# Kernel tuning notes

Hardware: AMD Instinct MI355X
Metric: run time of the kernel (lower is better)

The kernel has to match this reference:

```python
import jax, jax.numpy as jnp
import numpy as np

HID, H, DK, DV, PQK, PV = 128, 12, 16, 16, 4, 8
N, L = 4, 1024


def setup_inputs() -> dict:
    key = jax.random.key(0)
    ks = jax.random.split(key, 12)
    inp = {
        "x": jax.random.normal(ks[0], (N, L, HID), jnp.float32),
        "R": jax.random.normal(ks[1], (N, L, 3, 3), jnp.float32),
        "t": jax.random.normal(ks[2], (N, L, 3), jnp.float32),
        "mask": jnp.ones((N, L), dtype=bool),
        # Linear weights stored as (in, out) so y = x @ W
        "Wq": jax.random.normal(ks[3], (HID, H * DK), jnp.float32) * 0.05,
        "Wk": jax.random.normal(ks[4], (HID, H * DK), jnp.float32) * 0.05,
        "Wv": jax.random.normal(ks[5], (HID, H * DV), jnp.float32) * 0.05,
        "Wqv": jax.random.normal(ks[6], (HID, H * PQK * 3), jnp.float32) * 0.05,
        "Wkv": jax.random.normal(ks[7], (HID, H * PQK * 3), jnp.float32) * 0.05,
        "Wvv": jax.random.normal(ks[8], (HID, H * PV * 3), jnp.float32) * 0.05,
        "gamma": jax.random.normal(ks[9], (H,), jnp.float32) * 0.1,
        "Wo": jax.random.normal(ks[10], (H * (DV + PV * 4), HID), jnp.float32) * 0.05,
        "bo": jnp.zeros((HID,), jnp.float32),
    }
    return inp


def reference(x, R, t, mask, Wq, Wk, Wv, Wqv, Wkv, Wvv, gamma, Wo, bo):
    n, l, _ = x.shape
    q = (x @ Wq).reshape(n, l, H, DK)
    k = (x @ Wk).reshape(n, l, H, DK)
    # standard scores: (N,H,L,L)
    scores = jnp.einsum("bihd,bjhd->bhij", q, k) * DK ** -0.5

    q_vec = (x @ Wqv).reshape(n, l, H, PQK, 3)
    k_vec = (x @ Wkv).reshape(n, l, H, PQK, 3)
    # apply frame: R @ v + t, per residue i -> global frame points (N,L,H,P,3)
    qg = jnp.einsum("bixy,bihpy->bihpx", R, q_vec) + t[:, :, None, None, :]
    kg = jnp.einsum("bixy,bihpy->bihpx", R, k_vec) + t[:, :, None, None, :]
    # squared pairwise distance summed over points & xyz, via expansion
    # ||a-b||^2 = ||a||^2 + ||b||^2 - 2 a.b  (avoids (N,L,L,H,P,3) tensor)
    q2 = jnp.sum(qg * qg, axis=(-1, -2)).transpose(0, 2, 1)  # (N,H,L)
    k2 = jnp.sum(kg * kg, axis=(-1, -2)).transpose(0, 2, 1)
    cross = jnp.einsum("bihpc,bjhpc->bhij", qg, kg)
    d2 = (q2[:, :, :, None] + k2[:, :, None, :] - 2.0 * cross) * PQK ** -0.5

    att = 2 ** -0.5 * (scores - jax.nn.softplus(gamma)[None, :, None, None] * d2)
    diag = jnp.eye(l, dtype=bool)
    att = jnp.where(diag[None, None, :, :], jnp.float32(-100.0), att)
    att = jnp.where(mask[:, None, None, :], att, -jnp.inf)
    att = jax.nn.softmax(att, axis=-1)  # (N,H,L,L)

    v = (x @ Wv).reshape(n, l, H, DV)
    o = jnp.einsum("bhij,bjhd->bihd", att, v).reshape(n, l, H * DV)

    v_vec = (x @ Wvv).reshape(n, l, H, PV, 3)
    # frame-apply per key residue j: (N,H,L,P,3)
    vg = jnp.einsum("bjxy,bjhpy->bhjpx", R, v_vec) + t[:, None, :, None, :]
    o_vec = jnp.einsum("bhij,bhjpc->bihpc", att, vg).reshape(n, l, H * PV, 3)
    # inverse frame of query residue i: R^T (v - t)
    o_loc = jnp.einsum("bixy,bimx->bimy", R, o_vec - t[:, :, None, :])
    o_norm = jnp.linalg.norm(o_loc, axis=-1)  # (N,L,H*PV)

    feat = jnp.concatenate([o, o_loc.reshape(n, l, -1), o_norm], axis=-1)
    return feat @ Wo + bo
```

## Files before the change

### kernel.cpp

```cpp
#include <hip/hip_runtime.h>
#include <hip/hip_bf16.h>
#include <stdint.h>


#define NB 4
#define LL 1024
#define HH 12
#define NROW (NB*LL)
#define NHROW (NB*HH*LL)

typedef __attribute__((ext_vector_type(8))) short short8v;
typedef __attribute__((ext_vector_type(4))) float f32x4;

__device__ __forceinline__ ushort bf16rne(float x) {
    uint32_t u = __float_as_uint(x);
    return (ushort)((u + 0x7fffu + ((u >> 16) & 1u)) >> 16);
}
__device__ __forceinline__ ushort bf16trunc(float x) {
    return (ushort)(__float_as_uint(x) >> 16);
}
__device__ __forceinline__ float bf16tof(ushort h) {
    return __uint_as_float((uint32_t)h << 16);
}
__device__ __forceinline__ uint32_t pk2(ushort a, ushort b) {
    return (uint32_t)a | ((uint32_t)b << 16);
}
__device__ __forceinline__ void gload16(const void* g, void* l) {
    __builtin_amdgcn_global_load_lds(
        (const __attribute__((address_space(1))) void*)g,
        (__attribute__((address_space(3))) void*)(uint32_t)(uintptr_t)l,
        16, 0, 0);
}
__device__ __forceinline__ void split8(const float* f, short8v& h, short8v& l) {
    #pragma unroll
    for (int j = 0; j < 8; ++j) {
        const ushort hh = bf16trunc(f[j]);
        h[j] = (short)hh;
        l[j] = (short)bf16trunc(f[j] - bf16tof(hh));
    }
}

__global__ __launch_bounds__(256)
void k_prep(const float* __restrict__ Wq, const float* __restrict__ Wk,
            const float* __restrict__ Wv, const float* __restrict__ Wqv,
            const float* __restrict__ Wkv, const float* __restrict__ Wvv,
            const float* __restrict__ Wo,
            ushort* __restrict__ Wbh, ushort* __restrict__ Wbl,
            ushort* __restrict__ Wobh, ushort* __restrict__ Wobl)
{
    const int tid = blockIdx.x*256 + threadIdx.x;
    if (tid < 4*72*64) {
        const int lane = tid & 63, rest = tid >> 6;
        const int nc = rest % 72, ks = rest / 72;
        const int k0 = ks*32 + 8*(lane >> 4);
        const int col = nc*16 + (lane & 15);
        const float* W; int cc, wdt;
        if      (col < 192) { W = Wq;  cc = col;       wdt = 192; }
        else if (col < 384) { W = Wk;  cc = col - 192; wdt = 192; }
        else if (col < 576) { W = Wv;  cc = col - 384; wdt = 192; }
        else if (col < 720) { W = Wqv; cc = col - 576; wdt = 144; }
        else if (col < 864) { W = Wkv; cc = col - 720; wdt = 144; }
        else                { W = Wvv; cc = col - 864; wdt = 288; }
        #pragma unroll
        for (int j = 0; j < 8; ++j) {
            const float v = W[(size_t)(k0 + j)*wdt + cc];
            const ushort hh = bf16trunc(v);
            Wbh[(size_t)tid*8 + j] = hh;
            Wbl[(size_t)tid*8 + j] = bf16trunc(v - bf16tof(hh));
        }
    } else if (tid < 4*72*64 + 18*8*64) {
        const int t2 = tid - 4*72*64;
        const int lane = t2 & 63, rest = t2 >> 6;
        const int nc = rest % 8, ks = rest / 8;
        const int k0 = ks*32 + 8*(lane >> 4);
        const int col = nc*16 + (lane & 15);
        #pragma unroll
        for (int j = 0; j < 8; ++j) {
            const float v = Wo[(size_t)(k0 + j)*128 + col];
            const ushort hh = bf16trunc(v);
            Wobh[(size_t)t2*8 + j] = hh;
            Wobl[(size_t)t2*8 + j] = bf16trunc(v - bf16tof(hh));
        }
    }
}

__global__ __launch_bounds__(256)
void k_proj(const float* __restrict__ x,
            const ushort* __restrict__ Wbh, const ushort* __restrict__ Wbl,
            ushort* __restrict__ Qb, ushort* __restrict__ Kb,
            ushort* __restrict__ Vtb, float* __restrict__ raw)
{
    const int tid = threadIdx.x, lane = tid & 63, w = tid >> 6;
    const int l16 = lane & 15, g = lane >> 4;
    const int mblk = blockIdx.x & 63, nblk = blockIdx.x >> 6;
    const int m0 = mblk*64 + w*16;
    const int n0 = nblk*192;

    short8v ah[4], al[4];
    {
        const float* xp = x + (size_t)(m0 + l16)*128 + g*8;
        #pragma unroll
        for (int ks = 0; ks < 4; ++ks) {
            const float4 f0 = *reinterpret_cast<const float4*>(xp + ks*32);
            const float4 f1 = *reinterpret_cast<const float4*>(xp + ks*32 + 4);
            const float f[8] = {f0.x,f0.y,f0.z,f0.w,f1.x,f1.y,f1.z,f1.w};
            split8(f, ah[ks], al[ks]);
        }
    }

    const int rbase = m0 + 4*g;
    const int n = rbase >> 10, lp0 = rbase & 1023;

    #pragma unroll
    for (int nf = 0; nf < 12; ++nf) {
        const int nc = nblk*12 + nf;
        f32x4 acc = {0.f,0.f,0.f,0.f};
        #pragma unroll
        for (int ks = 0; ks < 4; ++ks) {
            const size_t bo_ = (((size_t)ks*72 + nc) << 9) + (lane << 3);
            const short8v bh = *reinterpret_cast<const short8v*>(Wbh + bo_);
            const short8v bl = *reinterpret_cast<const short8v*>(Wbl + bo_);
            acc = __builtin_amdgcn_mfma_f32_16x16x32_bf16(ah[ks], bh, acc, 0,0,0);
            acc = __builtin_amdgcn_mfma_f32_16x16x32_bf16(al[ks], bh, acc, 0,0,0);
            acc = __builtin_amdgcn_mfma_f32_16x16x32_bf16(ah[ks], bl, acc, 0,0,0);
        }
        const int c0 = n0 + nf*16;
        if (c0 < 192) {
            const int h = c0 >> 4;
            ushort* q = Qb + ((((size_t)(n*HH + h) << 10) + lp0) << 5) + l16;
            #pragma unroll
            for (int r = 0; r < 4; ++r)
                q[(size_t)r << 5] = bf16rne(0.25503492f*acc[r]);
        } else if (c0 < 384) {
            const int h = (c0 - 192) >> 4;
            ushort* k = Kb + ((((size_t)(n*HH + h) << 10) + lp0) << 5) + l16;
            #pragma unroll
            for (int r = 0; r < 4; ++r)
                k[(size_t)r << 5] = bf16rne(acc[r]);
        } else if (c0 < 576) {
            const int h = (c0 - 384) >> 4;
            ushort* v = Vtb + (((size_t)(n*HH + h)*48 + l16) << 10) + lp0;
            uint2 pk;
            pk.x = pk2(bf16rne(acc[0]), bf16rne(acc[1]));
            pk.y = pk2(bf16rne(acc[2]), bf16rne(acc[3]));
            *reinterpret_cast<uint2*>(v) = pk;
        } else {
            float* rp = raw + (size_t)rbase*576 + (c0 - 576) + l16;
            #pragma unroll
            for (int r = 0; r < 4; ++r) rp[(size_t)r*576] = acc[r];
        }
    }
}

__global__ __launch_bounds__(256)
void k_frames(const float* __restrict__ raw, const float* __restrict__ Rg,
              const float* __restrict__ tg, const float* __restrict__ gamma,
              ushort* __restrict__ Qb, ushort* __restrict__ Kb,
              ushort* __restrict__ Vtb)
{
    const int tid = blockIdx.x*256 + threadIdx.x;
    const int nh = tid >> 10, l = tid & 1023;
    const int h = nh % HH, n = nh / HH;
    const int xrow = (n << 10) | l;

    const float gm = gamma[h];
    const float sp = fmaxf(gm, 0.f) + log1pf(__expf(-fabsf(gm)));

    const float* Rm = Rg + (size_t)xrow*9;
    const float* tv = tg + (size_t)xrow*3;
    const float R00=Rm[0],R01=Rm[1],R02=Rm[2],
                R10=Rm[3],R11=Rm[4],R12=Rm[5],
                R20=Rm[6],R21=Rm[7],R22=Rm[8];
    const float t0=tv[0], t1=tv[1], t2=tv[2];

    const float* qv = raw + (size_t)xrow*576 +       h*12;
    const float* kv = raw + (size_t)xrow*576 + 144 + h*12;
    const float* vv = raw + (size_t)xrow*576 + 288 + h*24;

    ushort* Qr = Qb + (size_t)tid*32;
    ushort* Kr = Kb + (size_t)tid*32;

    const float cq = 1.02013944f * sp;
    ushort qh[16], kh[16];
    float q2 = 0.f;
    #pragma unroll
    for (int p = 0; p < 4; ++p) {
        const float y0=qv[p*3], y1=qv[p*3+1], y2=qv[p*3+2];
        const float gx = R00*y0+R01*y1+R02*y2+t0;
        const float gy = R10*y0+R11*y1+R12*y2+t1;
        const float gz = R20*y0+R21*y1+R22*y2+t2;
        q2 += gx*gx+gy*gy+gz*gz;
        qh[p*3+0]=bf16rne(cq*gx); qh[p*3+1]=bf16rne(cq*gy); qh[p*3+2]=bf16rne(cq*gz);
    }
    qh[12] = bf16rne(-0.51006972f*sp*q2);
    qh[13] = bf16rne(1.0f);
    qh[14] = bf16rne(1.0f);
    qh[15] = 0;

    float k2 = 0.f;
    #pragma unroll
    for (int p = 0; p < 4; ++p) {
        const float y0=kv[p*3], y1=kv[p*3+1], y2=kv[p*3+2];
        const float gx = R00*y0+R01*y1+R02*y2+t0;
        const float gy = R10*y0+R11*y1+R12*y2+t1;
        const float gz = R20*y0+R21*y1+R22*y2+t2;
        k2 += gx*gx+gy*gy+gz*gz;
        kh[p*3+0]=bf16rne(gx); kh[p*3+1]=bf16rne(gy); kh[p*3+2]=bf16rne(gz);
    }
    const float kc = -0.51006972f*sp*k2;
    const ushort hi = bf16rne(kc);
    const float hif = bf16tof(hi);
    kh[12] = bf16rne(1.0f);
    kh[13] = hi;
    kh[14] = bf16rne(kc - hif);
    kh[15] = 0;

    uint4 u;
    u.x=pk2(qh[0],qh[1]); u.y=pk2(qh[2],qh[3]); u.z=pk2(qh[4],qh[5]); u.w=pk2(qh[6],qh[7]);
    *reinterpret_cast<uint4*>(Qr+16) = u;
    u.x=pk2(qh[8],qh[9]); u.y=pk2(qh[10],qh[11]); u.z=pk2(qh[12],qh[13]); u.w=pk2(qh[14],qh[15]);
    *reinterpret_cast<uint4*>(Qr+24) = u;
    u.x=pk2(kh[0],kh[1]); u.y=pk2(kh[2],kh[3]); u.z=pk2(kh[4],kh[5]); u.w=pk2(kh[6],kh[7]);
    *reinterpret_cast<uint4*>(Kr+16) = u;
    u.x=pk2(kh[8],kh[9]); u.y=pk2(kh[10],kh[11]); u.z=pk2(kh[12],kh[13]); u.w=pk2(kh[14],kh[15]);
    *reinterpret_cast<uint4*>(Kr+24) = u;

    ushort* Vt = Vtb + (size_t)nh*48*1024 + l;
    #pragma unroll
    for (int p = 0; p < 8; ++p) {
        const float y0=vv[p*3], y1=vv[p*3+1], y2=vv[p*3+2];
        Vt[(size_t)(16+p*3+0)*1024] = bf16rne(R00*y0+R01*y1+R02*y2+t0);
        Vt[(size_t)(16+p*3+1)*1024] = bf16rne(R10*y0+R11*y1+R12*y2+t1);
        Vt[(size_t)(16+p*3+2)*1024] = bf16rne(R20*y0+R21*y1+R22*y2+t2);
    }
    #pragma unroll
    for (int d = 40; d < 48; ++d) Vt[(size_t)d*1024] = 0;
}

__global__ __launch_bounds__(256)
void k_attn(const ushort* __restrict__ Qb, const ushort* __restrict__ Kb,
            const ushort* __restrict__ Vtb, float* __restrict__ Og)
{
    __shared__ __align__(16) ushort Kbuf[2][2][1024];
    __shared__ __align__(16) ushort Vbuf[2][2][1536];
    __shared__ __align__(16) unsigned char Pl[4][1280];

    const int tid  = threadIdx.x;
    const int lane = tid & 63;
    const int w    = tid >> 6;
    const int lo   = lane & 15;
    const int g    = lane >> 4;
    const int bid  = blockIdx.x;
    const int nh   = bid % 48;
    const int qc   = bid / 48;
    const int qbase = qc*64 + w*16;
    const size_t rowbase = (size_t)nh << 10;

    const short8v qfrag = *reinterpret_cast<const short8v*>(
        Qb + ((rowbase + qbase + lo) << 5) + (g << 3));

    const ushort *sA, *sB = nullptr;
    int step;
    if (w == 0) {
        const int key = lane >> 2, gg = lane & 3, gp = gg ^ (key & 3);
        sA = Kb + ((rowbase + key) << 5) + (gp << 3);
        const int key2 = 16 + (lane >> 2), gp2 = gg ^ (key2 & 3);
        sB = Kb + ((rowbase + key2) << 5) + (gp2 << 3);
        step = 1024;
    } else {
        const int c = (w-1)*64 + lane;
        const int vd = c >> 2, gg = c & 3, gp = gg ^ (vd & 3);
        sA = Vtb + ((size_t)nh*48 + vd)*1024 + (gp << 3);
        step = 32;
    }
    const int vslot = (w-1)*512;

    #define STAGE(bb, it) do { \
        const int t0_ = 2*(it), t1_ = t0_ + 1; \
        if (w == 0) { \
            gload16(sA + (size_t)t0_*step, &Kbuf[bb][0][0]); \
            gload16(sB + (size_t)t0_*step, &Kbuf[bb][0][512]); \
            gload16(sA + (size_t)t1_*step, &Kbuf[bb][1][0]); \
            gload16(sB + (size_t)t1_*step, &Kbuf[bb][1][512]); \
        } else { \
            gload16(sA + (size_t)t0_*step, &Vbuf[bb][0][vslot]); \
            gload16(sA + (size_t)t1_*step, &Vbuf[bb][1][vslot]); \
        } \
    } while (0)

    f32x4 acc0 = {0.f,0.f,0.f,0.f}, acc1 = {0.f,0.f,0.f,0.f}, acc2 = {0.f,0.f,0.f,0.f};
    float m = -1e30f, lsum = 0.f;

    STAGE(0, 0);
    __syncthreads();

    const int usub = w >> 1;
    const int dsT  = w & 1;

    for (int t = 0; t < 16; ++t) {
        const int b = t & 1;
        if (t + 1 < 16) STAGE(b^1, t+1);

        #pragma unroll
        for (int u = 0; u < 2; ++u) {
            const char* kb = (const char*)&Kbuf[b][u][0];
            const char* vb = (const char*)&Vbuf[b][u][0];
            const f32x4 z = {0.f,0.f,0.f,0.f};

            f32x4 s0, s1;
            {
                int kk = lo;
                const short8v ka = *reinterpret_cast<const short8v*>(
                    kb + kk*64 + ((g*16) ^ ((kk&3)<<4)));
                s0 = __builtin_amdgcn_mfma_f32_16x16x32_bf16(ka, qfrag, z, 0, 0, 0);
                kk = 16 + lo;
                const short8v ka2 = *reinterpret_cast<const short8v*>(
                    kb + kk*64 + ((g*16) ^ ((kk&3)<<4)));
                s1 = __builtin_amdgcn_mfma_f32_16x16x32_bf16(ka2, qfrag, z, 0, 0, 0);
            }
            if (t == qc && u == usub) {
                #pragma unroll
                for (int r = 0; r < 4; ++r)
                    if (4*g + r == lo) { if (dsT == 0) s0[r] = -144.f; else s1[r] = -144.f; }
            }

            float tmax = fmaxf(fmaxf(fmaxf(s0[0],s0[1]),fmaxf(s0[2],s0[3])),
                               fmaxf(fmaxf(s1[0],s1[1]),fmaxf(s1[2],s1[3])));
            if (__any(tmax > m + 8.0f)) {
                float tq = tmax;
                tq = fmaxf(tq, __shfl_xor(tq, 16));
                tq = fmaxf(tq, __shfl_xor(tq, 32));
                const float mnew = fmaxf(m, tq);
                const float sc = exp2f(m - mnew);
                lsum *= sc;
                #pragma unroll
                for (int r = 0; r < 4; ++r) { acc0[r]*=sc; acc1[r]*=sc; acc2[r]*=sc; }
                m = mnew;
            }
            const float p0 = exp2f(s0[0]-m), p1 = exp2f(s0[1]-m);
            const float p2 = exp2f(s0[2]-m), p3 = exp2f(s0[3]-m);
            const float p4 = exp2f(s1[0]-m), p5 = exp2f(s1[1]-m);
            const float p6 = exp2f(s1[2]-m), p7 = exp2f(s1[3]-m);
            lsum += (((p0+p1)+(p2+p3)) + ((p4+p5)+(p6+p7)));

            unsigned char* pl = &Pl[w][0];
            uint2 wa, wb2;
            wa.x  = pk2(bf16trunc(p0), bf16trunc(p1));
            wa.y  = pk2(bf16trunc(p2), bf16trunc(p3));
            wb2.x = pk2(bf16trunc(p4), bf16trunc(p5));
            wb2.y = pk2(bf16trunc(p6), bf16trunc(p7));
            *reinterpret_cast<uint2*>(pl + lo*80 + g*8)      = wa;
            *reinterpret_cast<uint2*>(pl + lo*80 + 32 + g*8) = wb2;
            const short8v pfrag = *reinterpret_cast<const short8v*>(pl + lo*80 + g*16);

            {
                int row = lo;
                const short8v v0 = *reinterpret_cast<const short8v*>(
                    vb + row*64 + ((g*16) ^ ((row&3)<<4)));
                acc0 = __builtin_amdgcn_mfma_f32_16x16x32_bf16(v0, pfrag, acc0, 0,0,0);
                row = 16 + lo;
                const short8v v1 = *reinterpret_cast<const short8v*>(
                    vb + row*64 + ((g*16) ^ ((row&3)<<4)));
                acc1 = __builtin_amdgcn_mfma_f32_16x16x32_bf16(v1, pfrag, acc1, 0,0,0);
                row = 32 + lo;
                const short8v v2 = *reinterpret_cast<const short8v*>(
                    vb + row*64 + ((g*16) ^ ((row&3)<<4)));
                acc2 = __builtin_amdgcn_mfma_f32_16x16x32_bf16(v2, pfrag, acc2, 0,0,0);
            }
        }
        __syncthreads();
    }
    #undef STAGE

    lsum += __shfl_xor(lsum, 16);
    lsum += __shfl_xor(lsum, 32);
    const float inv = 1.0f / lsum;
    float* orow = Og + (rowbase + qbase + lo)*48;
    #pragma unroll
    for (int r = 0; r < 4; ++r) {
        orow[ 0 + 4*g + r] = acc0[r]*inv;
        orow[16 + 4*g + r] = acc1[r]*inv;
        orow[32 + 4*g + r] = acc2[r]*inv;
    }
}

__global__ __launch_bounds__(256)
void k_out(const float* __restrict__ Og, const float* __restrict__ Rg,
           const float* __restrict__ tg,
           const ushort* __restrict__ Wobh, const ushort* __restrict__ Wobl,
           const float* __restrict__ bo, float* __restrict__ out)
{
    __shared__ float fs[16*580];
    const int tid = threadIdx.x;
    const int m0 = blockIdx.x * 16;
    if (tid < 192) {
        const int row = tid & 15, h = tid >> 4;
        const int xrow = m0 + row, n = xrow >> 10, l = xrow & 1023;
        const float* og = Og + ((((size_t)(n*HH + h)) << 10) | l)*48;
        float o[48];
        #pragma unroll
        for (int u = 0; u < 12; ++u)
            *reinterpret_cast<float4*>(o + u*4) = *reinterpret_cast<const float4*>(og + u*4);
        const float* Rm = Rg + (size_t)xrow*9;
        const float* tv = tg + (size_t)xrow*3;
        const float R00=Rm[0],R01=Rm[1],R02=Rm[2],
                    R10=Rm[3],R11=Rm[4],R12=Rm[5],
                    R20=Rm[6],R21=Rm[7],R22=Rm[8];
        const float t0=tv[0], t1=tv[1], t2=tv[2];
        float* f = fs + row*580;
        #pragma unroll
        for (int d = 0; d < 16; ++d) f[h*16 + d] = o[d];
        #pragma unroll
        for (int p = 0; p < 8; ++p) {
            const float ux = o[16+p*3+0]-t0, uy = o[16+p*3+1]-t1, uz = o[16+p*3+2]-t2;
            const float lx = R00*ux + R10*uy + R20*uz;
            const float ly = R01*ux + R11*uy + R21*uz;
            const float lz = R02*ux + R12*uy + R22*uz;
            f[192 + (h*8+p)*3 + 0] = lx;
            f[192 + (h*8+p)*3 + 1] = ly;
            f[192 + (h*8+p)*3 + 2] = lz;
            f[480 + h*8 + p] = sqrtf(lx*lx + ly*ly + lz*lz);
        }
    }
    __syncthreads();
    {
        const int lane = tid & 63, w = tid >> 6;
        const int l16 = lane & 15, g = lane >> 4;
        const float* fpl = fs + l16*580 + g*8;

        f32x4 acc[2] = {{0.f,0.f,0.f,0.f},{0.f,0.f,0.f,0.f}};
        for (int ks = 0; ks < 18; ++ks) {
            const float4 f0 = *reinterpret_cast<const float4*>(fpl + ks*32);
            const float4 f1 = *reinterpret_cast<const float4*>(fpl + ks*32 + 4);
            const float f[8] = {f0.x,f0.y,f0.z,f0.w,f1.x,f1.y,f1.z,f1.w};
            short8v ah, al;
            split8(f, ah, al);
            #pragma unroll
            for (int nf = 0; nf < 2; ++nf) {
                const int nc = w*2 + nf;
                const size_t bo_ = (((size_t)ks*8 + nc) << 9) + (lane << 3);
                const short8v bh = *reinterpret_cast<const short8v*>(Wobh + bo_);
                const short8v bl = *reinterpret_cast<const short8v*>(Wobl + bo_);
                acc[nf] = __builtin_amdgcn_mfma_f32_16x16x32_bf16(ah, bh, acc[nf], 0,0,0);
                acc[nf] = __builtin_amdgcn_mfma_f32_16x16x32_bf16(al, bh, acc[nf], 0,0,0);
                acc[nf] = __builtin_amdgcn_mfma_f32_16x16x32_bf16(ah, bl, acc[nf], 0,0,0);
            }
        }
        const int rbase = m0 + 4*g;
        #pragma unroll
        for (int nf = 0; nf < 2; ++nf) {
            const int c = (w*2 + nf)*16 + l16;
            const float bias = bo[c];
            #pragma unroll
            for (int r = 0; r < 4; ++r)
                out[(size_t)(rbase + r)*128 + c] = acc[nf][r] + bias;
        }
    }
}

extern "C" void kernel_launch(void* const* d_in, const int* in_sizes, int n_in,
                              void* d_out, int out_size, void* d_ws, size_t ws_size,
                              hipStream_t stream)
{
    const float* x     = (const float*)d_in[0];
    const float* Rg    = (const float*)d_in[1];
    const float* tg    = (const float*)d_in[2];
    const float* Wq    = (const float*)d_in[4];
    const float* Wk    = (const float*)d_in[5];
    const float* Wv    = (const float*)d_in[6];
    const float* Wqv   = (const float*)d_in[7];
    const float* Wkv   = (const float*)d_in[8];
    const float* Wvv   = (const float*)d_in[9];
    const float* gamma = (const float*)d_in[10];
    const float* Wo    = (const float*)d_in[11];
    const float* bo    = (const float*)d_in[12];
    float* out = (float*)d_out;

    char* wsb = (char*)d_ws;
    ushort* Qb   = (ushort*)(wsb);
    ushort* Kb   = (ushort*)(wsb + 3145728);
    ushort* Vtb  = (ushort*)(wsb + 6291456);
    float*  raw  = (float*) (wsb + 11010048);
    float*  Og   = (float*) (wsb + 20447232);
    ushort* Wbh  = (ushort*)(wsb + 29884416);
    ushort* Wbl  = (ushort*)(wsb + 30179328);
    ushort* Wobh = (ushort*)(wsb + 30474240);
    ushort* Wobl = (ushort*)(wsb + 30621696);

    k_prep  <<<108, 256, 0, stream>>>(Wq, Wk, Wv, Wqv, Wkv, Wvv, Wo, Wbh, Wbl, Wobh, Wobl);
    k_proj  <<<384, 256, 0, stream>>>(x, Wbh, Wbl, Qb, Kb, Vtb, raw);
    k_frames<<<NHROW/256, 256, 0, stream>>>(raw, Rg, tg, gamma, Qb, Kb, Vtb);
    k_attn  <<<768, 256, 0, stream>>>(Qb, Kb, Vtb, Og);
    k_out   <<<NROW/16, 256, 0, stream>>>(Og, Rg, tg, Wobh, Wobl, bo, out);
}
```

Measured before the change: 81.86 us.

## Split attention key range into two halves and merge partials in output kernel

```diff
diff --git a/kernel.cpp b/kernel.cpp
--- a/kernel.cpp
+++ b/kernel.cpp
@@ -239,7 +239,7 @@
 
 __global__ __launch_bounds__(256)
 void k_attn(const ushort* __restrict__ Qb, const ushort* __restrict__ Kb,
-            const ushort* __restrict__ Vtb, float* __restrict__ Og)
+            const ushort* __restrict__ Vtb, float* __restrict__ part)
 {
     __shared__ __align__(16) ushort Kbuf[2][2][1024];
     __shared__ __align__(16) ushort Vbuf[2][2][1536];
@@ -252,7 +252,9 @@
     const int g    = lane >> 4;
     const int bid  = blockIdx.x;
     const int nh   = bid % 48;
-    const int qc   = bid / 48;
+    const int rest = bid / 48;
+    const int qc   = rest >> 1;
+    const int half = rest & 1;
     const int qbase = qc*64 + w*16;
     const size_t rowbase = (size_t)nh << 10;
 
@@ -274,9 +276,10 @@
         step = 32;
     }
     const int vslot = (w-1)*512;
+    const int sbase = half*16;
 
     #define STAGE(bb, it) do { \
-        const int t0_ = 2*(it), t1_ = t0_ + 1; \
+        const int t0_ = sbase + 2*(it), t1_ = t0_ + 1; \
         if (w == 0) { \
             gload16(sA + (size_t)t0_*step, &Kbuf[bb][0][0]); \
             gload16(sB + (size_t)t0_*step, &Kbuf[bb][0][512]); \
@@ -294,12 +297,12 @@
     STAGE(0, 0);
     __syncthreads();
 
-    const int usub = w >> 1;
-    const int dsT  = w & 1;
-
-    for (int t = 0; t < 16; ++t) {
+    const int dS  = 2*qc + (w >> 1) - sbase;
+    const int dsT = w & 1;
+
+    for (int t = 0; t < 8; ++t) {
         const int b = t & 1;
-        if (t + 1 < 16) STAGE(b^1, t+1);
+        if (t + 1 < 8) STAGE(b^1, t+1);
 
         #pragma unroll
         for (int u = 0; u < 2; ++u) {
@@ -318,7 +321,7 @@
                     kb + kk*64 + ((g*16) ^ ((kk&3)<<4)));
                 s1 = __builtin_amdgcn_mfma_f32_16x16x32_bf16(ka2, qfrag, z, 0, 0, 0);
             }
-            if (t == qc && u == usub) {
+            if ((unsigned)dS < 16u && (2*t + u) == dS) {
                 #pragma unroll
                 for (int r = 0; r < 4; ++r)
                     if (4*g + r == lo) { if (dsT == 0) s0[r] = -144.f; else s1[r] = -144.f; }
@@ -374,18 +377,23 @@
 
     lsum += __shfl_xor(lsum, 16);
     lsum += __shfl_xor(lsum, 32);
-    const float inv = 1.0f / lsum;
-    float* orow = Og + (rowbase + qbase + lo)*48;
+    float* orow = part + ((size_t)half*NHROW + rowbase + qbase + lo)*48;
     #pragma unroll
     for (int r = 0; r < 4; ++r) {
-        orow[ 0 + 4*g + r] = acc0[r]*inv;
-        orow[16 + 4*g + r] = acc1[r]*inv;
-        orow[32 + 4*g + r] = acc2[r]*inv;
+        orow[ 0 + 4*g + r] = acc0[r];
+        orow[16 + 4*g + r] = acc1[r];
+    }
+    if (g < 2) {
+        #pragma unroll
+        for (int r = 0; r < 4; ++r) orow[32 + 4*g + r] = acc2[r];
+    } else if (g == 2) {
+        orow[40] = m;
+        orow[41] = lsum;
     }
 }
 
 __global__ __launch_bounds__(256)
-void k_out(const float* __restrict__ Og, const float* __restrict__ Rg,
+void k_out(const float* __restrict__ part, const float* __restrict__ Rg,
            const float* __restrict__ tg,
            const ushort* __restrict__ Wobh, const ushort* __restrict__ Wobl,
            const float* __restrict__ bo, float* __restrict__ out)
@@ -396,11 +404,23 @@
     if (tid < 192) {
         const int row = tid & 15, h = tid >> 4;
         const int xrow = m0 + row, n = xrow >> 10, l = xrow & 1023;
-        const float* og = Og + ((((size_t)(n*HH + h)) << 10) | l)*48;
-        float o[48];
-        #pragma unroll
-        for (int u = 0; u < 12; ++u)
-            *reinterpret_cast<float4*>(o + u*4) = *reinterpret_cast<const float4*>(og + u*4);
+        const size_t rowg = (((size_t)(n*HH + h)) << 10) | l;
+        const float* pa = part + rowg*48;
+        const float* pb = part + ((size_t)NHROW + rowg)*48;
+        float oa[44], ob[44];
+        #pragma unroll
+        for (int u = 0; u < 11; ++u) {
+            *reinterpret_cast<float4*>(oa + u*4) = *reinterpret_cast<const float4*>(pa + u*4);
+            *reinterpret_cast<float4*>(ob + u*4) = *reinterpret_cast<const float4*>(pb + u*4);
+        }
+        const float m1 = oa[40], l1 = oa[41], m2 = ob[40], l2 = ob[41];
+        const float M  = fmaxf(m1, m2);
+        const float w1 = exp2f(m1 - M), w2 = exp2f(m2 - M);
+        const float inv = 1.0f / (w1*l1 + w2*l2);
+        float o[40];
+        #pragma unroll
+        for (int d = 0; d < 40; ++d) o[d] = (w1*oa[d] + w2*ob[d]) * inv;
+
         const float* Rm = Rg + (size_t)xrow*9;
         const float* tv = tg + (size_t)xrow*3;
         const float R00=Rm[0],R01=Rm[1],R02=Rm[2],
@@ -481,15 +501,15 @@
     ushort* Kb   = (ushort*)(wsb + 3145728);
     ushort* Vtb  = (ushort*)(wsb + 6291456);
     float*  raw  = (float*) (wsb + 11010048);
-    float*  Og   = (float*) (wsb + 20447232);
-    ushort* Wbh  = (ushort*)(wsb + 29884416);
-    ushort* Wbl  = (ushort*)(wsb + 30179328);
-    ushort* Wobh = (ushort*)(wsb + 30474240);
-    ushort* Wobl = (ushort*)(wsb + 30621696);
+    float*  part = (float*) (wsb + 20447232);
+    ushort* Wbh  = (ushort*)(wsb + 39321600);
+    ushort* Wbl  = (ushort*)(wsb + 39616512);
+    ushort* Wobh = (ushort*)(wsb + 39911424);
+    ushort* Wobl = (ushort*)(wsb + 40058880);
 
     k_prep  <<<108, 256, 0, stream>>>(Wq, Wk, Wv, Wqv, Wkv, Wvv, Wo, Wbh, Wbl, Wobh, Wobl);
     k_proj  <<<384, 256, 0, stream>>>(x, Wbh, Wbl, Qb, Kb, Vtb, raw);
     k_frames<<<NHROW/256, 256, 0, stream>>>(raw, Rg, tg, gamma, Qb, Kb, Vtb);
-    k_attn  <<<768, 256, 0, stream>>>(Qb, Kb, Vtb, Og);
-    k_out   <<<NROW/16, 256, 0, stream>>>(Og, Rg, tg, Wobh, Wobl, bo, out);
-}
+    k_attn  <<<1536, 256, 0, stream>>>(Qb, Kb, Vtb, part);
+    k_out   <<<NROW/16, 256, 0, stream>>>(part, Rg, tg, Wobh, Wobl, bo, out);
+}
```

New measurement: 79.63 us. -2.7%, faster.
